# Kernel optimization log

Hardware: AMD Instinct MI355X
Metric: run time of the kernel (lower is better)

The kernel has to match this reference:

```python
import jax, jax.numpy as jnp
import numpy as np

BINS = 10

def setup_inputs() -> dict:
    key = jax.random.key(0)
    k1, k2, k3 = jax.random.split(key, 3)
    shape = (8, 128, 128, 180)  # (batch, h, w, num_anchors*num_classes)
    class_labels = jax.random.randint(k1, shape, 0, 2, dtype=jnp.int32)
    class_logits = jax.random.normal(k2, shape, dtype=jnp.float32)
    label_weights = jax.random.uniform(k3, shape, dtype=jnp.float32)
    return {"class_labels": class_labels, "class_logits": class_logits,
            "label_weights": label_weights}


def reference(class_labels, class_logits, label_weights):
    bins = BINS
    probs = jax.nn.sigmoid(class_logits)
    labels_f = class_labels.astype(class_logits.dtype)
    # gradient magnitude proxy: |p - label|
    p_norm = jnp.where(class_labels == 1, 1.0 - probs, probs)
    total_num = jnp.maximum(jnp.sum(label_weights), 1.0)
    valid = (label_weights > 0).astype(class_logits.dtype)
    # bin edges are i/bins with last edge = 1 + 1e-6; sigmoid output is in (0,1)
    # so floor(p*bins) clipped to [0, bins-1] reproduces the bin assignment
    bin_idx = jnp.clip(jnp.floor(p_norm * bins).astype(jnp.int32), 0, bins - 1)
    counts = jax.ops.segment_sum(valid.ravel(), bin_idx.ravel(), num_segments=bins)
    n = jnp.sum(counts > 0).astype(class_logits.dtype)
    per_bin_w = jnp.where(counts > 0, total_num / jnp.maximum(counts, 1.0), 0.0)
    beta = per_bin_w[bin_idx] * valid
    beta = jnp.where(n > 0, beta / jnp.maximum(n, 1.0), beta)
    # tf.nn.sigmoid_cross_entropy_with_logits
    x = class_logits
    bce = jnp.maximum(x, 0.0) - x * labels_f + jnp.log1p(jnp.exp(-jnp.abs(x)))
    return jnp.sum(bce * beta) / total_num
```

## Files before the change

kernel.cpp:

```cpp
#include <hip/hip_runtime.h>
#include <math.h>

#define BINS 10
#define K1_THREADS 256
#define WPB   4
#define DEPTH 3
#define NSLOT 4
#define TILE  256
#define SLOT_BYTES 3072

__device__ __forceinline__ void ghm_elem(int y, float x, float w,
                                         float* __restrict__ G,
                                         float* __restrict__ C) {
    constexpr float TH[10] = {
        0.0f, -2.19722458f, -1.38629436f, -0.84729786f, -0.40546511f,
        0.0f,  0.40546511f,  0.84729786f,  1.38629436f,  2.19722458f };
    float xs = __int_as_float(__float_as_int(x) ^ (y << 31));
    bool  v  = (w > 0.0f);
    xs = v ? xs : -1e30f;
    C[0] += v ? 1.0f : 0.0f;
    float e   = __expf(-fabsf(xs));
    float bce = fmaxf(xs, 0.0f) + __logf(1.0f + e);
    G[0] += bce;
    #pragma unroll
    for (int b = 1; b < BINS; ++b) {
        bool ge = (xs >= TH[b]);
        C[b] += ge ? 1.0f : 0.0f;
        G[b] += ge ? bce : 0.0f;
    }
}

#define GLD_LDS16(gsrc, ldst)                                                  \
    __builtin_amdgcn_global_load_lds(                                          \
        (const __attribute__((address_space(1))) void*)(gsrc),                 \
        (__attribute__((address_space(3))) void*)(ldst), 16, 0, 0)

__global__ __launch_bounds__(K1_THREADS) void ghm_partial(
    const int*   __restrict__ labels,
    const float* __restrict__ logits,
    const float* __restrict__ weights,
    float*       __restrict__ partial,
    int NT, int n, int nb, int covered)
{
    __shared__ __align__(16) char ldsbuf[WPB][NSLOT][SLOT_BYTES];
    __shared__ float redc[WPB][BINS], redg[WPB][BINS];

    const int tid  = threadIdx.x;
    const int wid  = tid >> 6;
    const int lane = tid & 63;
    const int wgl  = blockIdx.x * WPB + wid;
    const int base0 = wgl * NT * TILE;

    float G[BINS], C[BINS];
    #pragma unroll
    for (int b = 0; b < BINS; ++b) { G[b] = 0.0f; C[b] = 0.0f; }

    const int*   labp = labels  + base0;
    const float* logp = logits  + base0;
    const float* wtp  = weights + base0;

    auto stage = [&](int k) {
        char* slot = &ldsbuf[wid][k & (NSLOT - 1)][0];
        const int off = k * TILE + lane * 4;
        GLD_LDS16(labp + off, slot);
        GLD_LDS16(logp + off, slot + 1024);
        GLD_LDS16(wtp  + off, slot + 2048);
    };
    auto consume = [&](int k) {
        const char* slot = &ldsbuf[wid][k & (NSLOT - 1)][0];
        int4   lb = *(const int4*)  (slot +        lane * 16);
        float4 xv = *(const float4*)(slot + 1024 + lane * 16);
        float4 wv = *(const float4*)(slot + 2048 + lane * 16);
        ghm_elem(lb.x, xv.x, wv.x, G, C);
        ghm_elem(lb.y, xv.y, wv.y, G, C);
        ghm_elem(lb.z, xv.z, wv.z, G, C);
        ghm_elem(lb.w, xv.w, wv.w, G, C);
    };

    if (NT > DEPTH) {
        stage(0); stage(1); stage(2);
        for (int t = 0; t < NT - DEPTH; ++t) {
            stage(t + DEPTH);
            asm volatile("s_waitcnt vmcnt(9)" ::: "memory");
            consume(t);
        }
        asm volatile("s_waitcnt vmcnt(6)" ::: "memory");
        consume(NT - 3);
        asm volatile("s_waitcnt vmcnt(3)" ::: "memory");
        consume(NT - 2);
        asm volatile("s_waitcnt vmcnt(0)" ::: "memory");
        consume(NT - 1);
    } else {
        for (int t = 0; t < NT; ++t) {
            stage(t);
            asm volatile("s_waitcnt vmcnt(0)" ::: "memory");
            consume(t);
        }
    }

    const int T = nb * K1_THREADS;
    for (int e2 = covered + blockIdx.x * K1_THREADS + tid; e2 < n; e2 += T)
        ghm_elem(labels[e2], logits[e2], weights[e2], G, C);

    #pragma unroll
    for (int off = 32; off > 0; off >>= 1) {
        #pragma unroll
        for (int b = 0; b < BINS; ++b) {
            C[b] += __shfl_down(C[b], off);
            G[b] += __shfl_down(G[b], off);
        }
    }
    if (lane == 0) {
        #pragma unroll
        for (int b = 0; b < BINS; ++b) { redc[wid][b] = C[b]; redg[wid][b] = G[b]; }
    }
    __syncthreads();
    if (tid < BINS) {
        float cc = 0.0f, gg = 0.0f;
        #pragma unroll
        for (int wv = 0; wv < WPB; ++wv) { cc += redc[wv][tid]; gg += redg[wv][tid]; }
        partial[tid * nb + blockIdx.x]          = cc;
        partial[(BINS + tid) * nb + blockIdx.x] = gg;
    }
}

__global__ __launch_bounds__(1024) void ghm_final(
    const float* __restrict__ partial, float* __restrict__ out, int nb)
{
    const int tid = threadIdx.x;
    float acc[2 * BINS];
    #pragma unroll
    for (int b = 0; b < 2 * BINS; ++b) acc[b] = 0.0f;
    for (int j = tid; j < nb; j += 1024) {
        #pragma unroll
        for (int b = 0; b < 2 * BINS; ++b)
            acc[b] += partial[b * nb + j];
    }
    #pragma unroll
    for (int off = 32; off > 0; off >>= 1) {
        #pragma unroll
        for (int b = 0; b < 2 * BINS; ++b)
            acc[b] += __shfl_down(acc[b], off);
    }
    __shared__ float red[16][2 * BINS];
    const int wave = tid >> 6, lane = tid & 63;
    if (lane == 0) {
        #pragma unroll
        for (int b = 0; b < 2 * BINS; ++b) red[wave][b] = acc[b];
    }
    __syncthreads();
    if (tid == 0) {
        float cum_c[BINS], cum_g[BINS];
        #pragma unroll
        for (int b = 0; b < BINS; ++b) { cum_c[b] = 0.0f; cum_g[b] = 0.0f; }
        for (int wv = 0; wv < 16; ++wv) {
            #pragma unroll
            for (int b = 0; b < BINS; ++b) {
                cum_c[b] += red[wv][b];
                cum_g[b] += red[wv][BINS + b];
            }
        }
        float nn = 0.0f, res = 0.0f;
        #pragma unroll
        for (int b = 0; b < BINS; ++b) {
            float Cb = (b < BINS - 1) ? (cum_c[b] - cum_c[b + 1]) : cum_c[b];
            float Sb = (b < BINS - 1) ? (cum_g[b] - cum_g[b + 1]) : cum_g[b];
            if (Cb > 0.5f) { nn += 1.0f; res += Sb / Cb; }
        }
        if (nn > 0.0f) res /= nn;
        out[0] = res;
    }
}

extern "C" void kernel_launch(void* const* d_in, const int* in_sizes, int n_in,
                              void* d_out, int out_size, void* d_ws, size_t ws_size,
                              hipStream_t stream) {
    const int*   labels  = (const int*)d_in[0];
    const float* logits  = (const float*)d_in[1];
    const float* weights = (const float*)d_in[2];
    float* out     = (float*)d_out;
    float* partial = (float*)d_ws;

    const int n = in_sizes[0];

    int nb = 1440;
    const size_t row_bytes = 2 * BINS * sizeof(float);
    if (ws_size < row_bytes * 1440) nb = 720;
    if (ws_size < row_bytes * 720)  nb = 360;

    const int NT      = n / (nb * WPB * TILE);
    const int covered = NT * nb * WPB * TILE;

    ghm_partial<<<nb, K1_THREADS, 0, stream>>>(labels, logits, weights, partial,
                                               NT, n, nb, covered);
    ghm_final<<<1, 1024, 0, stream>>>(partial, out, nb);
}
```

Measured before the change: 83.84 us.

## Replace LDS-staged loads with register triple-buffered direct global loads

Drops the global_load_lds staging through shared memory and instead issues inline-asm global_load_dwordx4 straight into registers, with three register buffers rotating and explicit vmcnt waits. The access pattern changes from per-wave contiguous chunks to a grid-strided layout, and launch_bounds now asks for 6 blocks per CU. The goal is to cut LDS round-trips and LDS capacity limits on occupancy. In exchange it raises register pressure, and the inline-asm loads depend on the sched_barrier to keep the compiler from reordering around them.

Measured after the change: 74.22 us. -11.5%, faster.

```diff
diff --git a/kernel.cpp b/kernel.cpp
--- a/kernel.cpp
+++ b/kernel.cpp
@@ -3,11 +3,9 @@
 
 #define BINS 10
 #define K1_THREADS 256
-#define WPB   4
-#define DEPTH 3
-#define NSLOT 4
-#define TILE  256
-#define SLOT_BYTES 3072
+
+typedef float f32x4 __attribute__((ext_vector_type(4)));
+typedef int   i32x4 __attribute__((ext_vector_type(4)));
 
 __device__ __forceinline__ void ghm_elem(int y, float x, float w,
                                          float* __restrict__ G,
@@ -30,76 +28,79 @@
     }
 }
 
-#define GLD_LDS16(gsrc, ldst)                                                  \
-    __builtin_amdgcn_global_load_lds(                                          \
-        (const __attribute__((address_space(1))) void*)(gsrc),                 \
-        (__attribute__((address_space(3))) void*)(ldst), 16, 0, 0)
-
-__global__ __launch_bounds__(K1_THREADS) void ghm_partial(
+#define GLOAD(dst, ptr) \
+    asm volatile("global_load_dwordx4 %0, %1, off" : "=v"(dst) : "v"(ptr))
+
+#define VMWAIT(N)                                              \
+    do { asm volatile("s_waitcnt vmcnt(" #N ")" ::: "memory"); \
+         __builtin_amdgcn_sched_barrier(0); } while (0)
+
+#define CONSUME(l, xv, wv)                        \
+    do {                                          \
+        ghm_elem(l[0], xv[0], wv[0], G, C);       \
+        ghm_elem(l[1], xv[1], wv[1], G, C);       \
+        ghm_elem(l[2], xv[2], wv[2], G, C);       \
+        ghm_elem(l[3], xv[3], wv[3], G, C);       \
+    } while (0)
+
+__global__ __launch_bounds__(K1_THREADS, 6) void ghm_partial(
     const int*   __restrict__ labels,
     const float* __restrict__ logits,
     const float* __restrict__ weights,
     float*       __restrict__ partial,
-    int NT, int n, int nb, int covered)
+    int n4, int n, int nb)
 {
-    __shared__ __align__(16) char ldsbuf[WPB][NSLOT][SLOT_BYTES];
-    __shared__ float redc[WPB][BINS], redg[WPB][BINS];
-
-    const int tid  = threadIdx.x;
-    const int wid  = tid >> 6;
-    const int lane = tid & 63;
-    const int wgl  = blockIdx.x * WPB + wid;
-    const int base0 = wgl * NT * TILE;
+    const int tid = blockIdx.x * K1_THREADS + threadIdx.x;
+    const int T   = gridDim.x * K1_THREADS;
 
     float G[BINS], C[BINS];
     #pragma unroll
     for (int b = 0; b < BINS; ++b) { G[b] = 0.0f; C[b] = 0.0f; }
 
-    const int*   labp = labels  + base0;
-    const float* logp = logits  + base0;
-    const float* wtp  = weights + base0;
-
-    auto stage = [&](int k) {
-        char* slot = &ldsbuf[wid][k & (NSLOT - 1)][0];
-        const int off = k * TILE + lane * 4;
-        GLD_LDS16(labp + off, slot);
-        GLD_LDS16(logp + off, slot + 1024);
-        GLD_LDS16(wtp  + off, slot + 2048);
-    };
-    auto consume = [&](int k) {
-        const char* slot = &ldsbuf[wid][k & (NSLOT - 1)][0];
-        int4   lb = *(const int4*)  (slot +        lane * 16);
-        float4 xv = *(const float4*)(slot + 1024 + lane * 16);
-        float4 wv = *(const float4*)(slot + 2048 + lane * 16);
-        ghm_elem(lb.x, xv.x, wv.x, G, C);
-        ghm_elem(lb.y, xv.y, wv.y, G, C);
-        ghm_elem(lb.z, xv.z, wv.z, G, C);
-        ghm_elem(lb.w, xv.w, wv.w, G, C);
-    };
-
-    if (NT > DEPTH) {
-        stage(0); stage(1); stage(2);
-        for (int t = 0; t < NT - DEPTH; ++t) {
-            stage(t + DEPTH);
-            asm volatile("s_waitcnt vmcnt(9)" ::: "memory");
-            consume(t);
-        }
-        asm volatile("s_waitcnt vmcnt(6)" ::: "memory");
-        consume(NT - 3);
-        asm volatile("s_waitcnt vmcnt(3)" ::: "memory");
-        consume(NT - 2);
-        asm volatile("s_waitcnt vmcnt(0)" ::: "memory");
-        consume(NT - 1);
-    } else {
-        for (int t = 0; t < NT; ++t) {
-            stage(t);
-            asm volatile("s_waitcnt vmcnt(0)" ::: "memory");
-            consume(t);
-        }
-    }
-
-    const int T = nb * K1_THREADS;
-    for (int e2 = covered + blockIdx.x * K1_THREADS + tid; e2 < n; e2 += T)
+    const i32x4* lab4 = (const i32x4*)labels;
+    const f32x4* log4 = (const f32x4*)logits;
+    const f32x4* w4   = (const f32x4*)weights;
+
+    const int nfull = n4 / T;
+    int consumed = 0;
+
+    if (nfull >= 3) {
+        i32x4 lA, lB, lC;
+        f32x4 xA, xB, xC, wA, wB, wC;
+        long ia = tid;
+        GLOAD(lA, lab4 + ia);         GLOAD(xA, log4 + ia);         GLOAD(wA, w4 + ia);
+        GLOAD(lB, lab4 + ia + T);     GLOAD(xB, log4 + ia + T);     GLOAD(wB, w4 + ia + T);
+        GLOAD(lC, lab4 + ia + 2*T);   GLOAD(xC, log4 + ia + 2*T);   GLOAD(wC, w4 + ia + 2*T);
+
+        const int s = (nfull - 3) / 3;
+        long inx = ia + 3L * T;
+        for (int it = 0; it < s; ++it) {
+            VMWAIT(6);
+            CONSUME(lA, xA, wA);
+            GLOAD(lA, lab4 + inx); GLOAD(xA, log4 + inx); GLOAD(wA, w4 + inx);
+            inx += T;
+            VMWAIT(6);
+            CONSUME(lB, xB, wB);
+            GLOAD(lB, lab4 + inx); GLOAD(xB, log4 + inx); GLOAD(wB, w4 + inx);
+            inx += T;
+            VMWAIT(6);
+            CONSUME(lC, xC, wC);
+            GLOAD(lC, lab4 + inx); GLOAD(xC, log4 + inx); GLOAD(wC, w4 + inx);
+            inx += T;
+        }
+        VMWAIT(6); CONSUME(lA, xA, wA);
+        VMWAIT(3); CONSUME(lB, xB, wB);
+        VMWAIT(0); CONSUME(lC, xC, wC);
+        consumed = 3 + 3 * s;
+    }
+
+    for (long i2 = (long)tid + (long)consumed * T; i2 < n4; i2 += T) {
+        i32x4 lb = lab4[i2];
+        f32x4 xv = log4[i2];
+        f32x4 wv = w4[i2];
+        CONSUME(lb, xv, wv);
+    }
+    for (int e2 = n4 * 4 + tid; e2 < n; e2 += T)
         ghm_elem(labels[e2], logits[e2], weights[e2], G, C);
 
     #pragma unroll
@@ -110,17 +111,23 @@
             G[b] += __shfl_down(G[b], off);
         }
     }
+    __shared__ float redc[K1_THREADS / 64][BINS];
+    __shared__ float redg[K1_THREADS / 64][BINS];
+    const int wid = threadIdx.x >> 6, lane = threadIdx.x & 63;
     if (lane == 0) {
         #pragma unroll
         for (int b = 0; b < BINS; ++b) { redc[wid][b] = C[b]; redg[wid][b] = G[b]; }
     }
     __syncthreads();
-    if (tid < BINS) {
+    if (threadIdx.x < BINS) {
         float cc = 0.0f, gg = 0.0f;
         #pragma unroll
-        for (int wv = 0; wv < WPB; ++wv) { cc += redc[wv][tid]; gg += redg[wv][tid]; }
-        partial[tid * nb + blockIdx.x]          = cc;
-        partial[(BINS + tid) * nb + blockIdx.x] = gg;
+        for (int wv = 0; wv < K1_THREADS / 64; ++wv) {
+            cc += redc[wv][threadIdx.x];
+            gg += redg[wv][threadIdx.x];
+        }
+        partial[threadIdx.x * nb + blockIdx.x]          = cc;
+        partial[(BINS + threadIdx.x) * nb + blockIdx.x] = gg;
     }
 }
 
@@ -181,17 +188,15 @@
     float* out     = (float*)d_out;
     float* partial = (float*)d_ws;
 
-    const int n = in_sizes[0];
+    const int n  = in_sizes[0];
+    const int n4 = n / 4;
 
     int nb = 1440;
     const size_t row_bytes = 2 * BINS * sizeof(float);
     if (ws_size < row_bytes * 1440) nb = 720;
     if (ws_size < row_bytes * 720)  nb = 360;
 
-    const int NT      = n / (nb * WPB * TILE);
-    const int covered = NT * nb * WPB * TILE;
-
     ghm_partial<<<nb, K1_THREADS, 0, stream>>>(labels, logits, weights, partial,
-                                               NT, n, nb, covered);
+                                               n4, n, nb);
     ghm_final<<<1, 1024, 0, stream>>>(partial, out, nb);
 }
```
